# Kernel tuning notes

Hardware: AMD Instinct MI355X
Metric: run time of the kernel (lower is better)

The kernel has to match this reference:

```python
import jax, jax.numpy as jnp
import numpy as np

MARGIN = 0.1
NEG_FLOOR = 0.6  # max(0.6, hardest_pos) threshold from the original code


def setup_inputs() -> dict:
    key = jax.random.key(0)
    k1, k2 = jax.random.split(key)
    n, d, n_classes = 8192, 128, 512
    emb = jax.random.normal(k1, (n, d), dtype=jnp.float32)
    target = jax.random.randint(k2, (n,), 0, n_classes, dtype=jnp.int64)
    return {"emb": emb, "target": target}


def reference(emb, target):
    n = emb.shape[0]
    # L2-normalize embeddings (F.normalize with eps=1e-12 clamp on the norm)
    norm = jnp.linalg.norm(emb, axis=-1, keepdims=True)
    e = emb / jnp.maximum(norm, 1e-12)
    sim = e @ e.T  # [n, n] cosine similarity

    same = target[:, None] == target[None, :]
    eye = jnp.eye(n, dtype=bool)
    pos_mask = same & ~eye
    neg_mask = ~same

    neg_inf = jnp.float32(-jnp.inf)
    # hardest (largest-sim) negative and positive per row; sorting in the
    # original only serves to grab these maxima and apply thresholds.
    max_neg = jnp.max(jnp.where(neg_mask, sim, neg_inf), axis=1)  # [n]
    max_pos = jnp.max(jnp.where(pos_mask, sim, neg_inf), axis=1)  # [n]

    has_pos = jnp.any(pos_mask, axis=1)  # rows with no positive contribute 0

    # positives with sim < hardest_neg + margin (hard positives)
    pos_sel = pos_mask & (sim < (max_neg + MARGIN)[:, None])
    pos_loss = jnp.sum(jnp.where(pos_sel, 1.0 - sim, 0.0), axis=1)

    # negatives with sim > max(0.6, hardest_pos) - margin (hard negatives)
    thr = jnp.maximum(jnp.float32(NEG_FLOOR), max_pos) - MARGIN
    neg_sel = neg_mask & (sim > thr[:, None])
    neg_loss = jnp.sum(jnp.where(neg_sel, sim, 0.0), axis=1)

    row_loss = jnp.where(has_pos, pos_loss + neg_loss, 0.0)
    return jnp.sum(row_loss) / n
```

## Files before the change

### kernel.cpp

```cpp
#include <hip/hip_runtime.h>


#define D 128
#define ROWG 2
#define SPLIT 64
#define NPART SPLIT
#define NCLS 512
#define CAP 2048
#define PSIM_CAP (512 * 1024)
#define MARGIN 0.1f
#define NEG_FLOOR 0.6f
#define NINF -1e30f

typedef short bf16x8 __attribute__((ext_vector_type(8)));
typedef float f32x4 __attribute__((ext_vector_type(4)));

__device__ __forceinline__ unsigned short f2bf(float f) {
  unsigned u = __float_as_uint(f);
  u += 0x7FFFu + ((u >> 16) & 1u);
  return (unsigned short)(u >> 16);
}

__device__ __forceinline__ void push_cand(unsigned* cnt,
                                          unsigned long long* cand, int row,
                                          float s) {
  unsigned idx = atomicAdd(cnt, 1u);
  if (idx < CAP)
    cand[idx] = ((unsigned long long)(unsigned)row << 32) | __float_as_uint(s);
}

__global__ void k_hist(const int* __restrict__ tgt, int* __restrict__ H,
                       unsigned* __restrict__ cnt) {
  if (blockIdx.x == 0 && threadIdx.x == 0) *cnt = 0u;
  __shared__ int h[NCLS];
  for (int i = threadIdx.x; i < NCLS; i += 128) h[i] = 0;
  __syncthreads();
  atomicAdd(&h[tgt[blockIdx.x * 128 + threadIdx.x]], 1);
  __syncthreads();
  for (int i = threadIdx.x; i < NCLS; i += 128)
    H[blockIdx.x * NCLS + i] = h[i];
}

__global__ void k_scan(const int* __restrict__ H, int* __restrict__ CB,
                       int* __restrict__ cls_start, int* __restrict__ pbase,
                       int n) {
  __shared__ int wsum[8], wsum2[8];
  const int c = threadIdx.x;
  int t = 0;
#pragma unroll 8
  for (int k = 0; k < 64; ++k) t += H[k * NCLS + c];
  const int t2 = t * t;
  const int lane = c & 63, w = c >> 6;
  int v = t, v2 = t2;
#pragma unroll
  for (int off = 1; off < 64; off <<= 1) {
    int u = __shfl_up(v, off, 64);
    int u2 = __shfl_up(v2, off, 64);
    if (lane >= off) {
      v += u;
      v2 += u2;
    }
  }
  if (lane == 63) {
    wsum[w] = v;
    wsum2[w] = v2;
  }
  __syncthreads();
  if (c < 8) {
    int x = wsum[c], x2 = wsum2[c];
#pragma unroll
    for (int off = 1; off < 8; off <<= 1) {
      int u = __shfl_up(x, off, 64);
      int u2 = __shfl_up(x2, off, 64);
      if (lane >= off) {
        x += u;
        x2 += u2;
      }
    }
    wsum[c] = x;
    wsum2[c] = x2;
  }
  __syncthreads();
  int base = v + ((w > 0) ? wsum[w - 1] : 0) - t;
  int base2 = v2 + ((w > 0) ? wsum2[w - 1] : 0) - t2;
  cls_start[c] = base;
  if (c == NCLS - 1) cls_start[NCLS] = n;
  pbase[c] = base2;
  int run = base;
#pragma unroll 8
  for (int k = 0; k < 64; ++k) {
    CB[k * NCLS + c] = run;
    run += H[k * NCLS + c];
  }
}

__global__ void k_scatter(const int* __restrict__ tgt,
                          const int* __restrict__ CB, int* __restrict__ perm) {
  const int c = threadIdx.x;
  int pos = CB[blockIdx.x * NCLS + c];
  const int base = blockIdx.x * 128;
  for (int j = 0; j < 128; ++j) {
    int cls = tgt[base + j];
    if (cls == c) perm[pos++] = base + j;
  }
}

__global__ void k_normB(const float* __restrict__ emb,
                        const int* __restrict__ tgt,
                        const int* __restrict__ perm,
                        const int* __restrict__ cls_start,
                        const int* __restrict__ pbase, uint4* __restrict__ ebB,
                        int* __restrict__ tgtS, int* __restrict__ rowS0,
                        int* __restrict__ rowM, int* __restrict__ rowBase,
                        int n) {
  const int s = blockIdx.x;
  const int rl = threadIdx.x >> 4;
  const int c = threadIdx.x & 15;
  const int p = s * 16 + rl;
  const int orig = perm[p];
  const float* q = emb + (size_t)orig * D + c * 8;
  float4 v0 = *(const float4*)q;
  float4 v1 = *(const float4*)(q + 4);
  float ss = v0.x * v0.x + v0.y * v0.y + v0.z * v0.z + v0.w * v0.w +
             v1.x * v1.x + v1.y * v1.y + v1.z * v1.z + v1.w * v1.w;
#pragma unroll
  for (int off = 1; off < 16; off <<= 1) ss += __shfl_xor(ss, off, 64);
  float invn = 1.0f / fmaxf(sqrtf(ss), 1e-12f);
  uint4 wv;
  wv.x = (unsigned)f2bf(v0.x * invn) | ((unsigned)f2bf(v0.y * invn) << 16);
  wv.y = (unsigned)f2bf(v0.z * invn) | ((unsigned)f2bf(v0.w * invn) << 16);
  wv.z = (unsigned)f2bf(v1.x * invn) | ((unsigned)f2bf(v1.y * invn) << 16);
  wv.w = (unsigned)f2bf(v1.z * invn) | ((unsigned)f2bf(v1.w * invn) << 16);
  const int ks = c >> 2, g = c & 3;
  ebB[((s * 4 + ks) * 64) + (g * 16 + rl)] = wv;
  if (c == 0) {
    int cls = tgt[orig];
    int s0 = cls_start[cls];
    tgtS[p] = cls;
    rowS0[p] = s0;
    rowM[p] = cls_start[cls + 1] - s0;
    rowBase[p] = pbase[cls];
  }
}

__global__ __launch_bounds__(256, 3) void k_passN(
    const bf16x8* __restrict__ ebB, const int* __restrict__ tgtS,
    const int* __restrict__ rowS0, const int* __restrict__ rowM,
    const int* __restrict__ rowBase, float* __restrict__ psim,
    float* __restrict__ mneg_p, unsigned* __restrict__ cnt,
    unsigned long long* __restrict__ cand, int n) {
  __shared__ char Bs[32768];

  const int lane = threadIdx.x & 63;
  const int w = threadIdx.x >> 6;
  const int l15 = lane & 15, g = lane >> 4;

  const int cs0 = blockIdx.y * 8;
  const int pidx = blockIdx.y;
  const int m0 = blockIdx.x * (128 * ROWG);

  {
    const char* src = (const char*)ebB + (size_t)cs0 * 4096;
#pragma unroll
    for (int i = 0; i < 8; ++i) {
      __builtin_amdgcn_global_load_lds(
          (const __attribute__((address_space(1))) void*)(src + i * 4096 +
                                                          threadIdx.x * 16),
          (__attribute__((address_space(3))) void*)(Bs + i * 4096 +
                                                    threadIdx.x * 16),
          16, 0, 0);
    }
  }
  int slo[8], shi[8];
#pragma unroll
  for (int si = 0; si < 8; ++si) {
    slo[si] = tgtS[(cs0 + si) * 16];
    shi[si] = tgtS[(cs0 + si) * 16 + 15];
  }
  __syncthreads();

#pragma unroll 1
  for (int p = 0; p < ROWG; ++p) {
    const int rbase = m0 + p * 128 + w * 32;
    const int sA = rbase >> 4;
    const int clo = tgtS[rbase], chi = tgtS[rbase + 31];

    bf16x8 a[2][4];
#pragma unroll
    for (int mt = 0; mt < 2; ++mt)
#pragma unroll
      for (int ks = 0; ks < 4; ++ks)
        a[mt][ks] = ebB[((sA + mt) * 4 + ks) * 64 + lane];

    float accN[2][4];
#pragma unroll
    for (int mt = 0; mt < 2; ++mt)
#pragma unroll
      for (int r = 0; r < 4; ++r) accN[mt][r] = NINF;

#pragma unroll
    for (int si = 0; si < 8; ++si) {
      bf16x8 b[4];
#pragma unroll
      for (int ks = 0; ks < 4; ++ks)
        b[ks] = *(const bf16x8*)(Bs + si * 4096 + ks * 1024 + lane * 16);
      const int cs = cs0 + si;
      const bool dirty = (clo <= shi[si]) && (slo[si] <= chi);

      f32x4 acc[2];
#pragma unroll
      for (int mt = 0; mt < 2; ++mt) acc[mt] = (f32x4){0.f, 0.f, 0.f, 0.f};
#pragma unroll
      for (int ks = 0; ks < 4; ++ks)
#pragma unroll
        for (int mt = 0; mt < 2; ++mt)
          acc[mt] = __builtin_amdgcn_mfma_f32_16x16x32_bf16(a[mt][ks], b[ks],
                                                            acc[mt], 0, 0, 0);
      if (!dirty) {
#pragma unroll
        for (int mt = 0; mt < 2; ++mt)
#pragma unroll
          for (int r = 0; r < 4; ++r)
            accN[mt][r] = fmaxf(accN[mt][r], acc[mt][r]);
        float m0x = fmaxf(fmaxf(acc[0][0], acc[0][1]),
                          fmaxf(acc[0][2], acc[0][3]));
        float m1x = fmaxf(fmaxf(acc[1][0], acc[1][1]),
                          fmaxf(acc[1][2], acc[1][3]));
        if (__any(fmaxf(m0x, m1x) > 0.5f)) {
#pragma unroll
          for (int mt = 0; mt < 2; ++mt)
#pragma unroll
            for (int r = 0; r < 4; ++r)
              if (acc[mt][r] > 0.5f)
                push_cand(cnt, cand, rbase + mt * 16 + g * 4 + r, acc[mt][r]);
        }
      } else {
        const int tc = tgtS[cs * 16 + l15];
        const int col = cs * 16 + l15;
        int4 ta = *(const int4*)(tgtS + rbase + g * 4);
        int4 tb = *(const int4*)(tgtS + rbase + 16 + g * 4);
        int tr[2][4] = {{ta.x, ta.y, ta.z, ta.w}, {tb.x, tb.y, tb.z, tb.w}};
#pragma unroll
        for (int mt = 0; mt < 2; ++mt)
#pragma unroll
          for (int r = 0; r < 4; ++r) {
            float s = acc[mt][r];
            const int row = rbase + mt * 16 + g * 4 + r;
            if (tr[mt][r] == tc) {
              int s0 = rowS0[row];
              int m = rowM[row];
              int b0 = rowBase[row];
              psim[b0 + (row - s0) * m + (col - s0)] = s;
            } else {
              accN[mt][r] = fmaxf(accN[mt][r], s);
              if (s > 0.5f) push_cand(cnt, cand, row, s);
            }
          }
      }
    }

#pragma unroll
    for (int mt = 0; mt < 2; ++mt)
#pragma unroll
      for (int r = 0; r < 4; ++r) {
        float vn = accN[mt][r];
#pragma unroll
        for (int off = 1; off < 16; off <<= 1)
          vn = fmaxf(vn, __shfl_xor(vn, off, 64));
        if (l15 == 0)
          mneg_p[(size_t)pidx * n + rbase + mt * 16 + g * 4 + r] = vn;
      }
  }
}

__global__ void k_combineN(const float* __restrict__ mneg_p,
                           float* __restrict__ thrPos,
                           float* __restrict__ negfix, int n) {
  int i = blockIdx.x * blockDim.x + threadIdx.x;
  if (i >= n) return;
  float vn = NINF;
#pragma unroll
  for (int s = 0; s < NPART; ++s) vn = fmaxf(vn, mneg_p[(size_t)s * n + i]);
  thrPos[i] = vn + MARGIN;
  negfix[i] = 0.f;
}

__global__ void k_posrow(const float* __restrict__ psim,
                         const int* __restrict__ rowS0,
                         const int* __restrict__ rowM,
                         const int* __restrict__ rowBase,
                         const float* __restrict__ thrPos,
                         float* __restrict__ thrNeg, float* __restrict__ posl,
                         float* __restrict__ hasp, int n) {
  int p = blockIdx.x * blockDim.x + threadIdx.x;
  if (p >= n) return;
  int m = rowM[p];
  if (m <= 1) {
    hasp[p] = 0.f;
    posl[p] = 0.f;
    thrNeg[p] = NEG_FLOOR - MARGIN;
    return;
  }
  int i = p - rowS0[p];
  const float* row = psim + rowBase[p] + (size_t)i * m;
  float tp = thrPos[p];
  float mp = NINF, pl = 0.f;
  for (int j = 0; j < m; ++j) {
    if (j == i) continue;
    float s = row[j];
    mp = fmaxf(mp, s);
    pl += (s < tp) ? (1.f - s) : 0.f;
  }
  hasp[p] = 1.f;
  posl[p] = pl;
  thrNeg[p] = fmaxf(NEG_FLOOR, mp) - MARGIN;
}

__global__ void k_fixup(const unsigned* __restrict__ cnt,
                        const unsigned long long* __restrict__ cand,
                        const float* __restrict__ thrNeg,
                        float* __restrict__ negfix) {
  __shared__ unsigned long long buf[CAP];
  __shared__ unsigned long long srt[CAP];
  int k = (int)min(*cnt, (unsigned)CAP);
  for (int i = threadIdx.x; i < k; i += 256) buf[i] = cand[i];
  __syncthreads();
  for (int i = threadIdx.x; i < k; i += 256) {
    unsigned long long v = buf[i];
    int rk = 0;
    for (int j = 0; j < k; ++j) {
      unsigned long long u = buf[j];
      rk += (u < v) || (u == v && j < i);
    }
    srt[rk] = v;
  }
  __syncthreads();
  if (threadIdx.x == 0) {
    for (int i = 0; i < k; ++i) {
      int row = (int)(srt[i] >> 32);
      float s = __uint_as_float((unsigned)srt[i]);
      if (s > thrNeg[row]) negfix[row] += s;
    }
  }
}

__global__ void k_final1(const float* __restrict__ posl,
                         const float* __restrict__ negfix,
                         const float* __restrict__ hasp,
                         float* __restrict__ bpart, int n) {
  __shared__ float red[256];
  int i = blockIdx.x * 256 + threadIdx.x;
  float acc = (hasp[i] != 0.f) ? (posl[i] + negfix[i]) : 0.f;
  red[threadIdx.x] = acc;
  __syncthreads();
  for (int off = 128; off > 0; off >>= 1) {
    if ((int)threadIdx.x < off) red[threadIdx.x] += red[threadIdx.x + off];
    __syncthreads();
  }
  if (threadIdx.x == 0) bpart[blockIdx.x] = red[0];
}

__global__ void k_final2(const float* __restrict__ bpart,
                         float* __restrict__ out, int n, int nb) {
  int lane = threadIdx.x & 63;
  float v = (lane < nb) ? bpart[lane] : 0.f;
#pragma unroll
  for (int off = 1; off < 64; off <<= 1) v += __shfl_xor(v, off, 64);
  if (lane == 0) out[0] = v / (float)n;
}

extern "C" void kernel_launch(void* const* d_in, const int* in_sizes, int n_in,
                              void* d_out, int out_size, void* d_ws,
                              size_t ws_size, hipStream_t stream) {
  const float* emb = (const float*)d_in[0];
  const int* tgt = (const int*)d_in[1];
  float* out = (float*)d_out;
  const int n = in_sizes[1];

  char* ws = (char*)d_ws;
  uint4* ebB = (uint4*)ws;
  float* mneg_p = (float*)(ws + (size_t)n * D * 2);
  float* psim = (float*)((char*)mneg_p + (size_t)NPART * n * 4);
  unsigned long long* cand = (unsigned long long*)(psim + PSIM_CAP);
  float* thrPos = (float*)(cand + CAP);
  float* thrNeg = thrPos + n;
  float* posl = thrNeg + n;
  float* negfix = posl + n;
  float* hasp = negfix + n;
  float* bpart = hasp + n;
  unsigned* cnt = (unsigned*)(bpart + 64);
  int* cls_start = (int*)(cnt + 64);
  int* pbase = cls_start + 1024;
  int* H = pbase + 1024;
  int* CB = H + 64 * NCLS;
  int* perm = CB + 64 * NCLS;
  int* tgtS = perm + n;
  int* rowS0 = tgtS + n;
  int* rowM = rowS0 + n;
  int* rowBase = rowM + n;

  k_hist<<<n / 128, 128, 0, stream>>>(tgt, H, cnt);
  k_scan<<<1, NCLS, 0, stream>>>(H, CB, cls_start, pbase, n);
  k_scatter<<<n / 128, NCLS, 0, stream>>>(tgt, CB, perm);
  k_normB<<<n / 16, 256, 0, stream>>>(emb, tgt, perm, cls_start, pbase, ebB,
                                      tgtS, rowS0, rowM, rowBase, n);

  dim3 grid(n / (128 * ROWG), SPLIT);
  k_passN<<<grid, 256, 0, stream>>>((const bf16x8*)ebB, tgtS, rowS0, rowM,
                                    rowBase, psim, mneg_p, cnt, cand, n);
  k_combineN<<<(n + 255) / 256, 256, 0, stream>>>(mneg_p, thrPos, negfix, n);
  k_posrow<<<(n + 255) / 256, 256, 0, stream>>>(psim, rowS0, rowM, rowBase,
                                                thrPos, thrNeg, posl, hasp, n);
  k_fixup<<<1, 256, 0, stream>>>(cnt, cand, thrNeg, negfix);
  k_final1<<<n / 256, 256, 0, stream>>>(posl, negfix, hasp, bpart, n);
  k_final2<<<1, 64, 0, stream>>>(bpart, out, n, n / 256);
}
```

Before: 72.07 us.

## Exploit similarity symmetry with upper-triangular tiles and atomic max-negative reduction

The similarity pass now covers only the upper-triangular block pairs and credits each off-diagonal tile to both its rows and its columns. Column maxima, mirrored positive-similarity writes and mirrored candidate pushes replace the lower half of the matrix, roughly halving MFMA work. The per-split partial max buffer and its combine kernel are replaced by order-preserving encoded atomicMax. The positive-row, fixup and final-reduction kernels are merged into fewer launches. The cost is extra atomics, doubled candidate pushes that may hit the CAP limit sooner, and a serial triangular index decode per block.

```diff
diff --git a/kernel.cpp b/kernel.cpp
--- a/kernel.cpp
+++ b/kernel.cpp
@@ -2,9 +2,6 @@
 
 
 #define D 128
-#define ROWG 2
-#define SPLIT 64
-#define NPART SPLIT
 #define NCLS 512
 #define CAP 2048
 #define PSIM_CAP (512 * 1024)
@@ -19,6 +16,15 @@
   unsigned u = __float_as_uint(f);
   u += 0x7FFFu + ((u >> 16) & 1u);
   return (unsigned short)(u >> 16);
+}
+
+__device__ __forceinline__ unsigned fenc(float f) {
+  unsigned u = __float_as_uint(f);
+  return (u & 0x80000000u) ? ~u : (u | 0x80000000u);
+}
+__device__ __forceinline__ float fdec(unsigned e) {
+  unsigned u = (e & 0x80000000u) ? (e & 0x7FFFFFFFu) : ~e;
+  return __uint_as_float(u);
 }
 
 __device__ __forceinline__ void push_cand(unsigned* cnt,
@@ -112,7 +118,7 @@
                         const int* __restrict__ pbase, uint4* __restrict__ ebB,
                         int* __restrict__ tgtS, int* __restrict__ rowS0,
                         int* __restrict__ rowM, int* __restrict__ rowBase,
-                        int n) {
+                        unsigned* __restrict__ maxNegEnc, int n) {
   const int s = blockIdx.x;
   const int rl = threadIdx.x >> 4;
   const int c = threadIdx.x & 15;
@@ -140,6 +146,7 @@
     rowS0[p] = s0;
     rowM[p] = cls_start[cls + 1] - s0;
     rowBase[p] = pbase[cls];
+    maxNegEnc[p] = 0u;
   }
 }
 
@@ -147,7 +154,7 @@
     const bf16x8* __restrict__ ebB, const int* __restrict__ tgtS,
     const int* __restrict__ rowS0, const int* __restrict__ rowM,
     const int* __restrict__ rowBase, float* __restrict__ psim,
-    float* __restrict__ mneg_p, unsigned* __restrict__ cnt,
+    unsigned* __restrict__ maxNegEnc, unsigned* __restrict__ cnt,
     unsigned long long* __restrict__ cand, int n) {
   __shared__ char Bs[32768];
 
@@ -155,9 +162,17 @@
   const int w = threadIdx.x >> 6;
   const int l15 = lane & 15, g = lane >> 4;
 
-  const int cs0 = blockIdx.y * 8;
-  const int pidx = blockIdx.y;
-  const int m0 = blockIdx.x * (128 * ROWG);
+  const int nby = n >> 7;
+  int t = blockIdx.x, bi = 0, rem = nby;
+  while (t >= rem) {
+    t -= rem;
+    ++bi;
+    rem -= 2;
+  }
+  const int bj = 2 * bi + t;
+  const bool colside = (bj >= 2 * bi + 2);
+  const int cs0 = bj * 8;
+  const int m0 = bi * 256;
 
   {
     const char* src = (const char*)ebB + (size_t)cs0 * 4096;
@@ -179,8 +194,12 @@
   }
   __syncthreads();
 
+  float accC[8];
+#pragma unroll
+  for (int si = 0; si < 8; ++si) accC[si] = NINF;
+
 #pragma unroll 1
-  for (int p = 0; p < ROWG; ++p) {
+  for (int p = 0; p < 2; ++p) {
     const int rbase = m0 + p * 128 + w * 32;
     const int sA = rbase >> 4;
     const int clo = tgtS[rbase], chi = tgtS[rbase + 31];
@@ -226,13 +245,19 @@
                           fmaxf(acc[0][2], acc[0][3]));
         float m1x = fmaxf(fmaxf(acc[1][0], acc[1][1]),
                           fmaxf(acc[1][2], acc[1][3]));
-        if (__any(fmaxf(m0x, m1x) > 0.5f)) {
+        float cm = fmaxf(m0x, m1x);
+        if (colside) accC[si] = fmaxf(accC[si], cm);
+        if (__any(cm > 0.5f)) {
 #pragma unroll
           for (int mt = 0; mt < 2; ++mt)
 #pragma unroll
             for (int r = 0; r < 4; ++r)
-              if (acc[mt][r] > 0.5f)
-                push_cand(cnt, cand, rbase + mt * 16 + g * 4 + r, acc[mt][r]);
+              if (acc[mt][r] > 0.5f) {
+                int row = rbase + mt * 16 + g * 4 + r;
+                int col = cs * 16 + l15;
+                push_cand(cnt, cand, row, acc[mt][r]);
+                if (colside) push_cand(cnt, cand, col, acc[mt][r]);
+              }
         }
       } else {
         const int tc = tgtS[cs * 16 + l15];
@@ -251,9 +276,14 @@
               int m = rowM[row];
               int b0 = rowBase[row];
               psim[b0 + (row - s0) * m + (col - s0)] = s;
+              if (colside) psim[b0 + (col - s0) * m + (row - s0)] = s;
             } else {
               accN[mt][r] = fmaxf(accN[mt][r], s);
-              if (s > 0.5f) push_cand(cnt, cand, row, s);
+              if (colside) accC[si] = fmaxf(accC[si], s);
+              if (s > 0.5f) {
+                push_cand(cnt, cand, row, s);
+                if (colside) push_cand(cnt, cand, col, s);
+              }
             }
           }
       }
@@ -268,58 +298,62 @@
         for (int off = 1; off < 16; off <<= 1)
           vn = fmaxf(vn, __shfl_xor(vn, off, 64));
         if (l15 == 0)
-          mneg_p[(size_t)pidx * n + rbase + mt * 16 + g * 4 + r] = vn;
+          atomicMax(&maxNegEnc[rbase + mt * 16 + g * 4 + r], fenc(vn));
       }
   }
-}
-
-__global__ void k_combineN(const float* __restrict__ mneg_p,
-                           float* __restrict__ thrPos,
-                           float* __restrict__ negfix, int n) {
-  int i = blockIdx.x * blockDim.x + threadIdx.x;
-  if (i >= n) return;
-  float vn = NINF;
-#pragma unroll
-  for (int s = 0; s < NPART; ++s) vn = fmaxf(vn, mneg_p[(size_t)s * n + i]);
-  thrPos[i] = vn + MARGIN;
-  negfix[i] = 0.f;
-}
-
-__global__ void k_posrow(const float* __restrict__ psim,
-                         const int* __restrict__ rowS0,
-                         const int* __restrict__ rowM,
-                         const int* __restrict__ rowBase,
-                         const float* __restrict__ thrPos,
-                         float* __restrict__ thrNeg, float* __restrict__ posl,
-                         float* __restrict__ hasp, int n) {
-  int p = blockIdx.x * blockDim.x + threadIdx.x;
-  if (p >= n) return;
+
+  if (colside) {
+#pragma unroll
+    for (int si = 0; si < 8; ++si) {
+      float v = accC[si];
+      v = fmaxf(v, __shfl_xor(v, 16, 64));
+      v = fmaxf(v, __shfl_xor(v, 32, 64));
+      if (g == 0) atomicMax(&maxNegEnc[(cs0 + si) * 16 + l15], fenc(v));
+    }
+  }
+}
+
+__global__ void k_stats(const float* __restrict__ psim,
+                        const int* __restrict__ rowS0,
+                        const int* __restrict__ rowM,
+                        const int* __restrict__ rowBase,
+                        const unsigned* __restrict__ maxNegEnc,
+                        float* __restrict__ thrNeg, float* __restrict__ bpart,
+                        int n) {
+  __shared__ float red[256];
+  int p = blockIdx.x * 256 + threadIdx.x;
+  float contrib = 0.f;
   int m = rowM[p];
   if (m <= 1) {
-    hasp[p] = 0.f;
-    posl[p] = 0.f;
-    thrNeg[p] = NEG_FLOOR - MARGIN;
-    return;
-  }
-  int i = p - rowS0[p];
-  const float* row = psim + rowBase[p] + (size_t)i * m;
-  float tp = thrPos[p];
-  float mp = NINF, pl = 0.f;
-  for (int j = 0; j < m; ++j) {
-    if (j == i) continue;
-    float s = row[j];
-    mp = fmaxf(mp, s);
-    pl += (s < tp) ? (1.f - s) : 0.f;
-  }
-  hasp[p] = 1.f;
-  posl[p] = pl;
-  thrNeg[p] = fmaxf(NEG_FLOOR, mp) - MARGIN;
-}
-
-__global__ void k_fixup(const unsigned* __restrict__ cnt,
-                        const unsigned long long* __restrict__ cand,
-                        const float* __restrict__ thrNeg,
-                        float* __restrict__ negfix) {
+    thrNeg[p] = 1e30f;
+  } else {
+    float tp = fdec(maxNegEnc[p]) + MARGIN;
+    int i = p - rowS0[p];
+    const float* row = psim + rowBase[p] + (size_t)i * m;
+    float mp = NINF, pl = 0.f;
+    for (int j = 0; j < m; ++j) {
+      if (j == i) continue;
+      float s = row[j];
+      mp = fmaxf(mp, s);
+      pl += (s < tp) ? (1.f - s) : 0.f;
+    }
+    thrNeg[p] = fmaxf(NEG_FLOOR, mp) - MARGIN;
+    contrib = pl;
+  }
+  red[threadIdx.x] = contrib;
+  __syncthreads();
+  for (int off = 128; off > 0; off >>= 1) {
+    if ((int)threadIdx.x < off) red[threadIdx.x] += red[threadIdx.x + off];
+    __syncthreads();
+  }
+  if (threadIdx.x == 0) bpart[blockIdx.x] = red[0];
+}
+
+__global__ void k_fix(const unsigned* __restrict__ cnt,
+                      const unsigned long long* __restrict__ cand,
+                      const float* __restrict__ thrNeg,
+                      const float* __restrict__ bpart, float* __restrict__ out,
+                      int n, int nb) {
   __shared__ unsigned long long buf[CAP];
   __shared__ unsigned long long srt[CAP];
   int k = (int)min(*cnt, (unsigned)CAP);
@@ -336,37 +370,15 @@
   }
   __syncthreads();
   if (threadIdx.x == 0) {
+    float tot = 0.f;
+    for (int i = 0; i < nb; ++i) tot += bpart[i];
     for (int i = 0; i < k; ++i) {
       int row = (int)(srt[i] >> 32);
       float s = __uint_as_float((unsigned)srt[i]);
-      if (s > thrNeg[row]) negfix[row] += s;
-    }
-  }
-}
-
-__global__ void k_final1(const float* __restrict__ posl,
-                         const float* __restrict__ negfix,
-                         const float* __restrict__ hasp,
-                         float* __restrict__ bpart, int n) {
-  __shared__ float red[256];
-  int i = blockIdx.x * 256 + threadIdx.x;
-  float acc = (hasp[i] != 0.f) ? (posl[i] + negfix[i]) : 0.f;
-  red[threadIdx.x] = acc;
-  __syncthreads();
-  for (int off = 128; off > 0; off >>= 1) {
-    if ((int)threadIdx.x < off) red[threadIdx.x] += red[threadIdx.x + off];
-    __syncthreads();
-  }
-  if (threadIdx.x == 0) bpart[blockIdx.x] = red[0];
-}
-
-__global__ void k_final2(const float* __restrict__ bpart,
-                         float* __restrict__ out, int n, int nb) {
-  int lane = threadIdx.x & 63;
-  float v = (lane < nb) ? bpart[lane] : 0.f;
-#pragma unroll
-  for (int off = 1; off < 64; off <<= 1) v += __shfl_xor(v, off, 64);
-  if (lane == 0) out[0] = v / (float)n;
+      if (s > thrNeg[row]) tot += s;
+    }
+    out[0] = tot / (float)n;
+  }
 }
 
 extern "C" void kernel_launch(void* const* d_in, const int* in_sizes, int n_in,
@@ -379,16 +391,12 @@
 
   char* ws = (char*)d_ws;
   uint4* ebB = (uint4*)ws;
-  float* mneg_p = (float*)(ws + (size_t)n * D * 2);
-  float* psim = (float*)((char*)mneg_p + (size_t)NPART * n * 4);
+  float* psim = (float*)(ws + (size_t)n * D * 2);
   unsigned long long* cand = (unsigned long long*)(psim + PSIM_CAP);
-  float* thrPos = (float*)(cand + CAP);
-  float* thrNeg = thrPos + n;
-  float* posl = thrNeg + n;
-  float* negfix = posl + n;
-  float* hasp = negfix + n;
-  float* bpart = hasp + n;
-  unsigned* cnt = (unsigned*)(bpart + 64);
+  float* thrNeg = (float*)(cand + CAP);
+  float* bpart = thrNeg + n;
+  unsigned* maxNegEnc = (unsigned*)(bpart + 64);
+  unsigned* cnt = maxNegEnc + n;
   int* cls_start = (int*)(cnt + 64);
   int* pbase = cls_start + 1024;
   int* H = pbase + 1024;
@@ -403,15 +411,15 @@
   k_scan<<<1, NCLS, 0, stream>>>(H, CB, cls_start, pbase, n);
   k_scatter<<<n / 128, NCLS, 0, stream>>>(tgt, CB, perm);
   k_normB<<<n / 16, 256, 0, stream>>>(emb, tgt, perm, cls_start, pbase, ebB,
-                                      tgtS, rowS0, rowM, rowBase, n);
-
-  dim3 grid(n / (128 * ROWG), SPLIT);
-  k_passN<<<grid, 256, 0, stream>>>((const bf16x8*)ebB, tgtS, rowS0, rowM,
-                                    rowBase, psim, mneg_p, cnt, cand, n);
-  k_combineN<<<(n + 255) / 256, 256, 0, stream>>>(mneg_p, thrPos, negfix, n);
-  k_posrow<<<(n + 255) / 256, 256, 0, stream>>>(psim, rowS0, rowM, rowBase,
-                                                thrPos, thrNeg, posl, hasp, n);
-  k_fixup<<<1, 256, 0, stream>>>(cnt, cand, thrNeg, negfix);
-  k_final1<<<n / 256, 256, 0, stream>>>(posl, negfix, hasp, bpart, n);
-  k_final2<<<1, 64, 0, stream>>>(bpart, out, n, n / 256);
-}
+                                      tgtS, rowS0, rowM, rowBase, maxNegEnc,
+                                      n);
+
+  const int nbx = n / 256, nby = n / 128;
+  const int tblocks = nbx * nby - nbx * (nbx - 1);
+  k_passN<<<tblocks, 256, 0, stream>>>((const bf16x8*)ebB, tgtS, rowS0, rowM,
+                                       rowBase, psim, maxNegEnc, cnt, cand,
+                                       n);
+  k_stats<<<n / 256, 256, 0, stream>>>(psim, rowS0, rowM, rowBase, maxNegEnc,
+                                       thrNeg, bpart, n);
+  k_fix<<<1, 256, 0, stream>>>(cnt, cand, thrNeg, bpart, out, n, n / 256);
+}
```

New measurement: 70.47 us. 2.2% less time.
